# Kernel optimization log

Hardware: AMD Instinct MI355X
Metric: run time of the kernel (lower is better)

## Reference

```python
import jax, jax.numpy as jnp
import numpy as np

B, N, D = 4, 4096, 256


def setup_inputs() -> dict:
    key = jax.random.key(0)
    k1, k2 = jax.random.split(key)
    val = jax.random.normal(k1, (B, N, D), dtype=jnp.float32)
    state = jax.random.normal(k2, (B, N), dtype=jnp.float32)
    return {"val": val, "state": state}


def reference(val, state):
    # pairwise_fn: scaled dot-product -> scores [B, N, N]
    scale = val.shape[-1] ** -0.5
    scores = jnp.einsum("bid,bjd->bij", val, val) * scale
    # edge_compress_fn = softsign (non-softmax compression)
    edges = scores / (1.0 + jnp.abs(scores))
    # state_weight_edges=False, val/state projections are Identity
    delta_state = jnp.einsum("bij,bj->bi", edges, state)   # [B, N]
    delta_val = jnp.einsum("bij,bjd->bid", edges, val)      # [B, N, D]
    return (delta_state, delta_val)
```

## Files before the change

kernel.cpp:

```cpp
#include <hip/hip_runtime.h>


#define B_  4
#define N_  4096
#define D_  256

typedef __attribute__((ext_vector_type(8))) short short8;
typedef __attribute__((ext_vector_type(4))) float floatx4;

__device__ __forceinline__ unsigned short f2bf(float f) {
    unsigned int u = __float_as_uint(f);
    u += 0x7fff + ((u >> 16) & 1);
    return (unsigned short)(u >> 16);
}

__device__ __forceinline__ void gl_lds16(const void* g, void* l) {
    __builtin_amdgcn_global_load_lds(
        (const __attribute__((address_space(1))) unsigned int*)g,
        (__attribute__((address_space(3))) unsigned int*)l, 16, 0, 0);
}
__device__ __forceinline__ void gl_lds4(const void* g, void* l) {
    __builtin_amdgcn_global_load_lds(
        (const __attribute__((address_space(1))) unsigned int*)g,
        (__attribute__((address_space(3))) unsigned int*)l, 4, 0, 0);
}

__global__ __launch_bounds__(256)
void prepass_kernel(const float* __restrict__ val,
                    unsigned short* __restrict__ Vb,
                    unsigned short* __restrict__ VF) {
    __shared__ unsigned short tile[64][68];
    const int t   = threadIdx.x;
    const int blk = blockIdx.x;
    const int b   = blk >> 8;
    const int it  = (blk >> 2) & 63;
    const int dt  = blk & 3;
    const int i0  = it * 64, d0 = dt * 64;
    const float*    vb  = val + (size_t)b * N_ * D_;
    unsigned short* Vbb = Vb  + (size_t)b * N_ * D_;
    unsigned short* VFb = VF  + (size_t)b * N_ * D_;

    #pragma unroll
    for (int q = 0; q < 4; ++q) {
        int idx = t + 256 * q;
        int row = idx >> 4;
        int c4  = idx & 15;
        float4 v = *(const float4*)(vb + (size_t)(i0 + row) * D_ + d0 + c4 * 4);
        ushort4 h;
        h.x = f2bf(v.x); h.y = f2bf(v.y); h.z = f2bf(v.z); h.w = f2bf(v.w);
        *(ushort4*)(Vbb + (size_t)(i0 + row) * D_ + d0 + c4 * 4) = h;
        *(ushort4*)&tile[row][c4 * 4] = h;
    }
    __syncthreads();
    #pragma unroll
    for (int q = 0; q < 4; ++q) {
        int dr = (t >> 4) + q * 16;
        int i4 = t & 15;
        ushort4 h;
        h.x = tile[i4 * 4 + 0][dr];
        h.y = tile[i4 * 4 + 1][dr];
        h.z = tile[i4 * 4 + 2][dr];
        h.w = tile[i4 * 4 + 3][dr];
        const int jb = (i0 >> 5) + (i4 >> 3);
        const int e  = (i4 & 7) * 4;
        *(ushort4*)(VFb + ((size_t)jb * 256 + d0 + dr) * 32 + e) = h;
    }
}

__global__ __launch_bounds__(256, 2)
void prop_main(const float* __restrict__ state,
               const unsigned short* __restrict__ Vb,
               const unsigned short* __restrict__ VF,
               float* __restrict__ dvp,
               float* __restrict__ dsp_o)
{
    __shared__ __attribute__((aligned(16))) unsigned char smem[74752];

    const int t    = threadIdx.x;
    const int w    = t >> 6;
    const int lane = t & 63;
    const int quad = lane >> 4;
    const int l16  = lane & 15;

    const int x   = blockIdx.x;
    const int it  = x >> 3;
    const int b   = (x >> 1) & 3;
    const int jh  = x & 1;
    const int it0 = it * 64;
    const int jbase = jh * 2048;
    const int niter = 32;

    unsigned short* EshL = (unsigned short*)(smem + 65536);
    float*          dsred = (float*)(smem + 74240);

    const unsigned short* Vbb = Vb + (size_t)b * N_ * D_;
    const unsigned short* VFb = VF + (size_t)b * N_ * D_;
    const float*          stb = state + (size_t)b * N_;

    const int hi  = lane >> 5;
    const int p32 = lane & 31;

    int vgoff[8];
    #pragma unroll
    for (int n = 0; n < 8; ++n) {
        int r  = 2 * (w * 8 + n) + hi;
        int gr = p32 ^ (r & 7);
        vgoff[n] = r * 256 + gr * 8;
    }

    const int r0 = (w >> 1) * 32;
    const int c0 = (w & 1) * 32;
    const int pA = l16 & 7;
    const int cB = (w & 1) * 4 + (l16 >> 3);
    const int l7 = l16 & 7;

    const unsigned short* vf_lane = VFb + (size_t)jh * (64 * 8192)
                                  + w * 2048 + l16 * 32 + quad * 8;

    short8 A0[8], A1[8];
    {
        const unsigned short* ar0 = Vbb + (size_t)(it0 + r0 + l16) * 256 + quad * 8;
        const unsigned short* ar1 = ar0 + 16 * 256;
        #pragma unroll
        for (int ks = 0; ks < 8; ++ks) {
            A0[ks] = *(const short8*)(ar0 + ks * 32);
            A1[ks] = *(const short8*)(ar1 + ks * 32);
        }
    }

    #pragma unroll
    for (int n = 0; n < 8; ++n)
        gl_lds16(Vbb + (size_t)jbase * 256 + vgoff[n],
                 smem + (w * 8 + n) * 1024);
    if (w == 0) gl_lds4(stb + jbase + lane, smem + 73728);

    floatx4 dv[4][4];
    #pragma unroll
    for (int a = 0; a < 4; ++a)
        #pragma unroll
        for (int c = 0; c < 4; ++c)
            dv[a][c] = (floatx4){0.f, 0.f, 0.f, 0.f};
    float dsp[8];
    #pragma unroll
    for (int k = 0; k < 8; ++k) dsp[k] = 0.f;

    for (int k = 0; k < niter; ++k) {
        const int buf = k & 1;
        unsigned short* vjL = (unsigned short*)(smem + buf * 32768);
        const float*    stj = (const float*)(smem + 73728 + buf * 256);

        __syncthreads();

        short8 bfr[2][4];
        {
            const unsigned short* vfk = vf_lane + (size_t)k * 16384;
            #pragma unroll
            for (int ks = 0; ks < 2; ++ks)
                #pragma unroll
                for (int c2 = 0; c2 < 4; ++c2)
                    bfr[ks][c2] = *(const short8*)(vfk + ks * 8192 + c2 * 512);
        }

        if (k + 1 < niter) {
            const size_t j0n = jbase + (size_t)(k + 1) * 64;
            #pragma unroll
            for (int n = 0; n < 8; ++n)
                gl_lds16(Vbb + j0n * 256 + vgoff[n],
                         smem + (buf ^ 1) * 32768 + (w * 8 + n) * 1024);
            if (w == 0) gl_lds4(stb + j0n + lane, smem + 73728 + (buf ^ 1) * 256);
        }

        floatx4 sa[2][2];
        #pragma unroll
        for (int a = 0; a < 2; ++a)
            #pragma unroll
            for (int c = 0; c < 2; ++c)
                sa[a][c] = (floatx4){0.f, 0.f, 0.f, 0.f};

        #pragma unroll
        for (int ks = 0; ks < 8; ++ks) {
            const int p = ((ks * 4 + quad) ^ pA) * 8;
            short8 b0 = *(const short8*)&vjL[(c0 + l16) * 256 + p];
            short8 b1 = *(const short8*)&vjL[(c0 + 16 + l16) * 256 + p];
            sa[0][0] = __builtin_amdgcn_mfma_f32_16x16x32_bf16(A0[ks], b0, sa[0][0], 0, 0, 0);
            sa[0][1] = __builtin_amdgcn_mfma_f32_16x16x32_bf16(A0[ks], b1, sa[0][1], 0, 0, 0);
            sa[1][0] = __builtin_amdgcn_mfma_f32_16x16x32_bf16(A1[ks], b0, sa[1][0], 0, 0, 0);
            sa[1][1] = __builtin_amdgcn_mfma_f32_16x16x32_bf16(A1[ks], b1, sa[1][1], 0, 0, 0);
        }

        float stc0 = stj[c0 + l16];
        float stc1 = stj[c0 + 16 + l16];
        #pragma unroll
        for (int a = 0; a < 2; ++a) {
            #pragma unroll
            for (int r = 0; r < 4; ++r) {
                const int il  = r0 + a * 16 + quad * 4 + r;
                const int ilb = (quad * 4 + r) & 7;
                float s0 = sa[a][0][r];
                float s1 = sa[a][1][r];
                float e0 = s0 * __builtin_amdgcn_rcpf(16.0f + fabsf(s0));
                float e1 = s1 * __builtin_amdgcn_rcpf(16.0f + fabsf(s1));
                dsp[a * 4 + r] += e0 * stc0 + e1 * stc1;
                EshL[il * 64 + ((cB ^ ilb) << 3) + l7]       = f2bf(e0);
                EshL[il * 64 + (((cB + 2) ^ ilb) << 3) + l7] = f2bf(e1);
            }
        }
        __syncthreads();

        #pragma unroll
        for (int ks = 0; ks < 2; ++ks) {
            short8 af[4];
            #pragma unroll
            for (int a2 = 0; a2 < 4; ++a2)
                af[a2] = *(const short8*)&EshL[(a2 * 16 + l16) * 64
                                               + (((ks * 4 + quad) ^ l7) << 3)];
            #pragma unroll
            for (int a2 = 0; a2 < 4; ++a2)
                #pragma unroll
                for (int c2 = 0; c2 < 4; ++c2)
                    dv[a2][c2] = __builtin_amdgcn_mfma_f32_16x16x32_bf16(af[a2], bfr[ks][c2], dv[a2][c2], 0, 0, 0);
        }
    }

    float* dvo = dvp + (size_t)jh * B_ * N_ * D_ + (size_t)b * N_ * D_
                     + (size_t)it0 * D_;
    #pragma unroll
    for (int a2 = 0; a2 < 4; ++a2)
        #pragma unroll
        for (int c2 = 0; c2 < 4; ++c2)
            #pragma unroll
            for (int r = 0; r < 4; ++r) {
                const int il = a2 * 16 + quad * 4 + r;
                const int d  = w * 64 + c2 * 16 + l16;
                dvo[(size_t)il * D_ + d] = dv[a2][c2][r];
            }

    #pragma unroll
    for (int k = 0; k < 8; ++k) {
        float v = dsp[k];
        v += __shfl_xor(v, 1);
        v += __shfl_xor(v, 2);
        v += __shfl_xor(v, 4);
        v += __shfl_xor(v, 8);
        dsp[k] = v;
    }
    if (l16 == 0) {
        #pragma unroll
        for (int a = 0; a < 2; ++a)
            #pragma unroll
            for (int r = 0; r < 4; ++r) {
                const int row = r0 + a * 16 + quad * 4 + r;
                dsred[(w & 1) * 64 + row] = dsp[a * 4 + r];
            }
    }
    __syncthreads();
    if (t < 64)
        dsp_o[(size_t)jh * B_ * N_ + (size_t)b * N_ + it0 + t]
            = dsred[t] + dsred[64 + t];
}

__global__ __launch_bounds__(256)
void combine_kernel(const float4* __restrict__ dv0, const float4* __restrict__ dv1,
                    const float*  __restrict__ ds0, const float*  __restrict__ ds1,
                    float* __restrict__ out) {
    const int NDV4 = B_ * N_ * D_ / 4;
    const int NDS  = B_ * N_;
    int x = blockIdx.x * 256 + threadIdx.x;
    if (x < NDV4) {
        float4 a = dv0[x], c = dv1[x];
        float4 r;
        r.x = a.x + c.x; r.y = a.y + c.y; r.z = a.z + c.z; r.w = a.w + c.w;
        ((float4*)(out + NDS))[x] = r;
    } else {
        int y = (x - NDV4) * 4;
        if (y < NDS) {
            float4 a = *(const float4*)(ds0 + y);
            float4 c = *(const float4*)(ds1 + y);
            float4 r;
            r.x = a.x + c.x; r.y = a.y + c.y; r.z = a.z + c.z; r.w = a.w + c.w;
            *(float4*)(out + y) = r;
        }
    }
}

__global__ __launch_bounds__(256, 1)
void prop_kernel_fb(const float* __restrict__ val,
                    const float* __restrict__ state,
                    float* __restrict__ out) {
    __shared__ __attribute__((aligned(16))) unsigned short vi[64][264];
    __shared__ __attribute__((aligned(16))) unsigned short vj[64][264];
    __shared__ __attribute__((aligned(16))) unsigned short vjt[2048][8];
    __shared__ __attribute__((aligned(16))) unsigned short Esh[64][72];
    __shared__ float stj[64];
    __shared__ float dsred[2][64];

    const int t    = threadIdx.x;
    const int w    = t >> 6;
    const int lane = t & 63;
    const int quad = lane >> 4;
    const int l16  = lane & 15;
    const int b   = blockIdx.x >> 6;
    const int it0 = (blockIdx.x & 63) << 6;
    const float* valb = val   + (size_t)b * N_ * D_;
    const float* stb  = state + (size_t)b * N_;

    #pragma unroll
    for (int n = 0; n < 16; ++n) {
        int idx = t + 256 * n;
        int row = idx >> 6;
        int c4  = idx & 63;
        float4 v = *(const float4*)(valb + (size_t)(it0 + row) * D_ + c4 * 4);
        ushort4 h;
        h.x = f2bf(v.x); h.y = f2bf(v.y); h.z = f2bf(v.z); h.w = f2bf(v.w);
        *(ushort4*)&vi[row][c4 * 4] = h;
    }

    const int r0 = (w >> 1) * 32;
    const int c0 = (w & 1) * 32;
    floatx4 dv[4][4];
    #pragma unroll
    for (int a = 0; a < 4; ++a)
        #pragma unroll
        for (int c = 0; c < 4; ++c)
            dv[a][c] = (floatx4){0.f, 0.f, 0.f, 0.f};
    float dsp[8];
    #pragma unroll
    for (int k = 0; k < 8; ++k) dsp[k] = 0.f;

    for (int jt = 0; jt < 64; ++jt) {
        const int j0 = jt * 64;
        #pragma unroll
        for (int n = 0; n < 16; ++n) {
            int idx = t + 256 * n;
            int row = idx >> 6;
            int c4  = idx & 63;
            float4 v = *(const float4*)(valb + (size_t)(j0 + row) * D_ + c4 * 4);
            ushort4 h;
            h.x = f2bf(v.x); h.y = f2bf(v.y); h.z = f2bf(v.z); h.w = f2bf(v.w);
            *(ushort4*)&vj[row][c4 * 4] = h;
        }
        if (t < 64) stj[t] = stb[j0 + t];
        __syncthreads();

        #pragma unroll
        for (int n = 0; n < 8; ++n) {
            const int d  = t;
            const int jb = n;
            short8 pk;
            #pragma unroll
            for (int jj = 0; jj < 8; ++jj) pk[jj] = (short)vj[jb * 8 + jj][d];
            *(short8*)&vjt[d * 8 + (jb ^ (d & 7))][0] = pk;
        }

        floatx4 sa[2][2];
        #pragma unroll
        for (int a = 0; a < 2; ++a)
            #pragma unroll
            for (int c = 0; c < 2; ++c)
                sa[a][c] = (floatx4){0.f, 0.f, 0.f, 0.f};
        #pragma unroll
        for (int ks = 0; ks < 8; ++ks) {
            const int d0 = ks * 32 + quad * 8;
            short8 a0 = *(const short8*)&vi[r0 + l16][d0];
            short8 a1 = *(const short8*)&vi[r0 + 16 + l16][d0];
            short8 b0 = *(const short8*)&vj[c0 + l16][d0];
            short8 b1 = *(const short8*)&vj[c0 + 16 + l16][d0];
            sa[0][0] = __builtin_amdgcn_mfma_f32_16x16x32_bf16(a0, b0, sa[0][0], 0, 0, 0);
            sa[0][1] = __builtin_amdgcn_mfma_f32_16x16x32_bf16(a0, b1, sa[0][1], 0, 0, 0);
            sa[1][0] = __builtin_amdgcn_mfma_f32_16x16x32_bf16(a1, b0, sa[1][0], 0, 0, 0);
            sa[1][1] = __builtin_amdgcn_mfma_f32_16x16x32_bf16(a1, b1, sa[1][1], 0, 0, 0);
        }

        float stc0 = stj[c0 + l16];
        float stc1 = stj[c0 + 16 + l16];
        #pragma unroll
        for (int a = 0; a < 2; ++a) {
            #pragma unroll
            for (int r = 0; r < 4; ++r) {
                const int il = r0 + a * 16 + quad * 4 + r;
                float s0 = sa[a][0][r] * 0.0625f;
                float s1 = sa[a][1][r] * 0.0625f;
                float e0 = s0 / (1.0f + fabsf(s0));
                float e1 = s1 / (1.0f + fabsf(s1));
                dsp[a * 4 + r] += e0 * stc0 + e1 * stc1;
                Esh[il][c0 + l16]      = f2bf(e0);
                Esh[il][c0 + 16 + l16] = f2bf(e1);
            }
        }
        __syncthreads();

        #pragma unroll
        for (int ks = 0; ks < 2; ++ks) {
            short8 af[4], bfr[4];
            #pragma unroll
            for (int a2 = 0; a2 < 4; ++a2)
                af[a2] = *(const short8*)&Esh[a2 * 16 + l16][ks * 32 + quad * 8];
            #pragma unroll
            for (int c2 = 0; c2 < 4; ++c2) {
                const int d  = w * 64 + c2 * 16 + l16;
                const int jb = ks * 4 + quad;
                bfr[c2] = *(const short8*)&vjt[d * 8 + (jb ^ (d & 7))][0];
            }
            #pragma unroll
            for (int a2 = 0; a2 < 4; ++a2)
                #pragma unroll
                for (int c2 = 0; c2 < 4; ++c2)
                    dv[a2][c2] = __builtin_amdgcn_mfma_f32_16x16x32_bf16(af[a2], bfr[c2], dv[a2][c2], 0, 0, 0);
        }
    }

    float* dvo = out + (size_t)B_ * N_ + (size_t)b * N_ * D_;
    #pragma unroll
    for (int a2 = 0; a2 < 4; ++a2)
        #pragma unroll
        for (int c2 = 0; c2 < 4; ++c2)
            #pragma unroll
            for (int r = 0; r < 4; ++r) {
                const int i = it0 + a2 * 16 + quad * 4 + r;
                const int d = w * 64 + c2 * 16 + l16;
                dvo[(size_t)i * D_ + d] = dv[a2][c2][r];
            }

    #pragma unroll
    for (int k = 0; k < 8; ++k) {
        float v = dsp[k];
        v += __shfl_xor(v, 1);
        v += __shfl_xor(v, 2);
        v += __shfl_xor(v, 4);
        v += __shfl_xor(v, 8);
        dsp[k] = v;
    }
    if (l16 == 0) {
        #pragma unroll
        for (int a = 0; a < 2; ++a)
            #pragma unroll
            for (int r = 0; r < 4; ++r) {
                const int row = (w >> 1) * 32 + a * 16 + quad * 4 + r;
                dsred[w & 1][row] = dsp[a * 4 + r];
            }
    }
    __syncthreads();
    if (t < 64) out[(size_t)b * N_ + it0 + t] = dsred[0][t] + dsred[1][t];
}

extern "C" void kernel_launch(void* const* d_in, const int* in_sizes, int n_in,
                              void* d_out, int out_size, void* d_ws, size_t ws_size,
                              hipStream_t stream) {
    const float* val   = (const float*)d_in[0];
    const float* state = (const float*)d_in[1];
    float* out = (float*)d_out;

    const size_t nE         = (size_t)B_ * N_ * D_;
    const size_t need_base  = 2 * nE * sizeof(unsigned short);
    const size_t need_split = need_base + 2 * nE * sizeof(float)
                            + 2 * (size_t)B_ * N_ * sizeof(float);

    if (ws_size >= need_split) {
        unsigned short* Vb = (unsigned short*)d_ws;
        unsigned short* VF = Vb + nE;
        float* dvp = (float*)(VF + nE);
        float* dsp = dvp + 2 * nE;
        prepass_kernel<<<dim3(1024), dim3(256), 0, stream>>>(val, Vb, VF);
        prop_main<<<dim3(512), dim3(256), 0, stream>>>(state, Vb, VF, dvp, dsp);
        const int NDV4 = B_ * N_ * D_ / 4;
        const int NDS4 = B_ * N_ / 4;
        combine_kernel<<<dim3((NDV4 + NDS4) / 256), dim3(256), 0, stream>>>(
            (const float4*)dvp, (const float4*)(dvp + nE),
            dsp, dsp + (size_t)B_ * N_, out);
    } else {
        prop_kernel_fb<<<dim3(256), dim3(256), 0, stream>>>(val, state, out);
    }
}
```

Before: 155.1 us.

## Split j-range into four parts with bf16 partials and single-buffered LDS

The j dimension is split into four quarters instead of two, doubling the grid to 1024 blocks. LDS is cut to a single V buffer plus the edge tile so that four blocks can fit per CU. The V tile prefetch now runs after the edge-write barrier instead of double buffering, and state values are read straight from global memory. Partial dv/ds results are stored as bf16 to halve partial-sum traffic, and the combine kernel sums four bf16 partials. The trade-off is less load/compute overlap within a block and extra rounding error from the bf16 partials.

```diff
diff --git a/kernel.cpp b/kernel.cpp
--- a/kernel.cpp
+++ b/kernel.cpp
@@ -6,6 +6,7 @@
 #define D_  256
 
 typedef __attribute__((ext_vector_type(8))) short short8;
+typedef __attribute__((ext_vector_type(8))) unsigned short ushort8v;
 typedef __attribute__((ext_vector_type(4))) float floatx4;
 
 __device__ __forceinline__ unsigned short f2bf(float f) {
@@ -13,16 +14,14 @@
     u += 0x7fff + ((u >> 16) & 1);
     return (unsigned short)(u >> 16);
 }
+__device__ __forceinline__ float bf2f(unsigned short h) {
+    return __uint_as_float((unsigned int)h << 16);
+}
 
 __device__ __forceinline__ void gl_lds16(const void* g, void* l) {
     __builtin_amdgcn_global_load_lds(
         (const __attribute__((address_space(1))) unsigned int*)g,
         (__attribute__((address_space(3))) unsigned int*)l, 16, 0, 0);
-}
-__device__ __forceinline__ void gl_lds4(const void* g, void* l) {
-    __builtin_amdgcn_global_load_lds(
-        (const __attribute__((address_space(1))) unsigned int*)g,
-        (__attribute__((address_space(3))) unsigned int*)l, 4, 0, 0);
 }
 
 __global__ __launch_bounds__(256)
@@ -67,31 +66,32 @@
     }
 }
 
-__global__ __launch_bounds__(256, 2)
+__global__ __launch_bounds__(256, 4)
 void prop_main(const float* __restrict__ state,
                const unsigned short* __restrict__ Vb,
                const unsigned short* __restrict__ VF,
-               float* __restrict__ dvp,
-               float* __restrict__ dsp_o)
+               unsigned short* __restrict__ dvp,
+               unsigned short* __restrict__ dsp_o)
 {
-    __shared__ __attribute__((aligned(16))) unsigned char smem[74752];
+    __shared__ __attribute__((aligned(16))) unsigned char smem[40960];
 
     const int t    = threadIdx.x;
     const int w    = t >> 6;
     const int lane = t & 63;
     const int quad = lane >> 4;
     const int l16  = lane & 15;
+    const int l7   = lane & 7;
 
     const int x   = blockIdx.x;
-    const int it  = x >> 3;
     const int b   = (x >> 1) & 3;
-    const int jh  = x & 1;
+    const int jq  = (x & 1) * 2 + ((x >> 3) & 1);
+    const int it  = x >> 4;
     const int it0 = it * 64;
-    const int jbase = jh * 2048;
-    const int niter = 32;
-
-    unsigned short* EshL = (unsigned short*)(smem + 65536);
-    float*          dsred = (float*)(smem + 74240);
+    const int jbase = jq * 1024;
+    const int niter = 16;
+
+    unsigned short* vjL  = (unsigned short*)smem;
+    unsigned short* EshL = (unsigned short*)(smem + 32768);
 
     const unsigned short* Vbb = Vb + (size_t)b * N_ * D_;
     const unsigned short* VFb = VF + (size_t)b * N_ * D_;
@@ -110,12 +110,10 @@
 
     const int r0 = (w >> 1) * 32;
     const int c0 = (w & 1) * 32;
-    const int pA = l16 & 7;
     const int cB = (w & 1) * 4 + (l16 >> 3);
-    const int l7 = l16 & 7;
-
-    const unsigned short* vf_lane = VFb + (size_t)jh * (64 * 8192)
-                                  + w * 2048 + l16 * 32 + quad * 8;
+
+    const unsigned short* vf_lane = VFb + (size_t)jq * 32 * 8192
+                                  + (w * 64 + l16) * 32 + quad * 8;
 
     short8 A0[8], A1[8];
     {
@@ -132,7 +130,6 @@
     for (int n = 0; n < 8; ++n)
         gl_lds16(Vbb + (size_t)jbase * 256 + vgoff[n],
                  smem + (w * 8 + n) * 1024);
-    if (w == 0) gl_lds4(stb + jbase + lane, smem + 73728);
 
     floatx4 dv[4][4];
     #pragma unroll
@@ -145,11 +142,11 @@
     for (int k = 0; k < 8; ++k) dsp[k] = 0.f;
 
     for (int k = 0; k < niter; ++k) {
-        const int buf = k & 1;
-        unsigned short* vjL = (unsigned short*)(smem + buf * 32768);
-        const float*    stj = (const float*)(smem + 73728 + buf * 256);
-
         __syncthreads();
+
+        const int j0 = jbase + k * 64;
+        float stc0 = stb[j0 + c0 + l16];
+        float stc1 = stb[j0 + c0 + 16 + l16];
 
         short8 bfr[2][4];
         {
@@ -161,15 +158,6 @@
                     bfr[ks][c2] = *(const short8*)(vfk + ks * 8192 + c2 * 512);
         }
 
-        if (k + 1 < niter) {
-            const size_t j0n = jbase + (size_t)(k + 1) * 64;
-            #pragma unroll
-            for (int n = 0; n < 8; ++n)
-                gl_lds16(Vbb + j0n * 256 + vgoff[n],
-                         smem + (buf ^ 1) * 32768 + (w * 8 + n) * 1024);
-            if (w == 0) gl_lds4(stb + j0n + lane, smem + 73728 + (buf ^ 1) * 256);
-        }
-
         floatx4 sa[2][2];
         #pragma unroll
         for (int a = 0; a < 2; ++a)
@@ -179,7 +167,7 @@
 
         #pragma unroll
         for (int ks = 0; ks < 8; ++ks) {
-            const int p = ((ks * 4 + quad) ^ pA) * 8;
+            const int p = ((ks * 4 + quad) ^ l7) * 8;
             short8 b0 = *(const short8*)&vjL[(c0 + l16) * 256 + p];
             short8 b1 = *(const short8*)&vjL[(c0 + 16 + l16) * 256 + p];
             sa[0][0] = __builtin_amdgcn_mfma_f32_16x16x32_bf16(A0[ks], b0, sa[0][0], 0, 0, 0);
@@ -188,8 +176,6 @@
             sa[1][1] = __builtin_amdgcn_mfma_f32_16x16x32_bf16(A1[ks], b1, sa[1][1], 0, 0, 0);
         }
 
-        float stc0 = stj[c0 + l16];
-        float stc1 = stj[c0 + 16 + l16];
         #pragma unroll
         for (int a = 0; a < 2; ++a) {
             #pragma unroll
@@ -207,6 +193,14 @@
         }
         __syncthreads();
 
+        if (k + 1 < niter) {
+            const size_t j0n = (size_t)(jbase + (k + 1) * 64);
+            #pragma unroll
+            for (int n = 0; n < 8; ++n)
+                gl_lds16(Vbb + j0n * 256 + vgoff[n],
+                         smem + (w * 8 + n) * 1024);
+        }
+
         #pragma unroll
         for (int ks = 0; ks < 2; ++ks) {
             short8 af[4];
@@ -222,8 +216,8 @@
         }
     }
 
-    float* dvo = dvp + (size_t)jh * B_ * N_ * D_ + (size_t)b * N_ * D_
-                     + (size_t)it0 * D_;
+    unsigned short* dvo = dvp + ((size_t)jq * B_ + b) * N_ * D_
+                        + (size_t)it0 * D_;
     #pragma unroll
     for (int a2 = 0; a2 < 4; ++a2)
         #pragma unroll
@@ -232,9 +226,10 @@
             for (int r = 0; r < 4; ++r) {
                 const int il = a2 * 16 + quad * 4 + r;
                 const int d  = w * 64 + c2 * 16 + l16;
-                dvo[(size_t)il * D_ + d] = dv[a2][c2][r];
-            }
-
+                dvo[(size_t)il * D_ + d] = f2bf(dv[a2][c2][r]);
+            }
+
+    float* dsred = (float*)smem;
     #pragma unroll
     for (int k = 0; k < 8; ++k) {
         float v = dsp[k];
@@ -255,29 +250,44 @@
     }
     __syncthreads();
     if (t < 64)
-        dsp_o[(size_t)jh * B_ * N_ + (size_t)b * N_ + it0 + t]
-            = dsred[t] + dsred[64 + t];
+        dsp_o[(size_t)jq * B_ * N_ + (size_t)b * N_ + it0 + t]
+            = f2bf(dsred[t] + dsred[64 + t]);
 }
 
 __global__ __launch_bounds__(256)
-void combine_kernel(const float4* __restrict__ dv0, const float4* __restrict__ dv1,
-                    const float*  __restrict__ ds0, const float*  __restrict__ ds1,
+void combine_kernel(const unsigned short* __restrict__ dvp,
+                    const unsigned short* __restrict__ dsp,
                     float* __restrict__ out) {
-    const int NDV4 = B_ * N_ * D_ / 4;
-    const int NDS  = B_ * N_;
+    const size_t nE  = (size_t)B_ * N_ * D_;
+    const int  NDV8  = B_ * N_ * D_ / 8;
+    const int  NDS   = B_ * N_;
     int x = blockIdx.x * 256 + threadIdx.x;
-    if (x < NDV4) {
-        float4 a = dv0[x], c = dv1[x];
-        float4 r;
-        r.x = a.x + c.x; r.y = a.y + c.y; r.z = a.z + c.z; r.w = a.w + c.w;
-        ((float4*)(out + NDS))[x] = r;
+    if (x < NDV8) {
+        float acc[8];
+        #pragma unroll
+        for (int i = 0; i < 8; ++i) acc[i] = 0.f;
+        #pragma unroll
+        for (int q = 0; q < 4; ++q) {
+            ushort8v v = *(const ushort8v*)(dvp + q * nE + (size_t)x * 8);
+            #pragma unroll
+            for (int i = 0; i < 8; ++i) acc[i] += bf2f(v[i]);
+        }
+        float4 r0, r1;
+        r0.x = acc[0]; r0.y = acc[1]; r0.z = acc[2]; r0.w = acc[3];
+        r1.x = acc[4]; r1.y = acc[5]; r1.z = acc[6]; r1.w = acc[7];
+        *(float4*)(out + NDS + (size_t)x * 8)     = r0;
+        *(float4*)(out + NDS + (size_t)x * 8 + 4) = r1;
     } else {
-        int y = (x - NDV4) * 4;
+        int y = (x - NDV8) * 4;
         if (y < NDS) {
-            float4 a = *(const float4*)(ds0 + y);
-            float4 c = *(const float4*)(ds1 + y);
-            float4 r;
-            r.x = a.x + c.x; r.y = a.y + c.y; r.z = a.z + c.z; r.w = a.w + c.w;
+            float a0 = 0.f, a1 = 0.f, a2 = 0.f, a3 = 0.f;
+            #pragma unroll
+            for (int q = 0; q < 4; ++q) {
+                ushort4 v = *(const ushort4*)(dsp + q * NDS + y);
+                a0 += bf2f(v.x); a1 += bf2f(v.y);
+                a2 += bf2f(v.z); a3 += bf2f(v.w);
+            }
+            float4 r; r.x = a0; r.y = a1; r.z = a2; r.w = a3;
             *(float4*)(out + y) = r;
         }
     }
@@ -451,22 +461,21 @@
     float* out = (float*)d_out;
 
     const size_t nE         = (size_t)B_ * N_ * D_;
-    const size_t need_base  = 2 * nE * sizeof(unsigned short);
-    const size_t need_split = need_base + 2 * nE * sizeof(float)
-                            + 2 * (size_t)B_ * N_ * sizeof(float);
+    const size_t need_split = 2 * nE * sizeof(unsigned short)
+                            + 4 * nE * sizeof(unsigned short)
+                            + 4 * (size_t)B_ * N_ * sizeof(unsigned short);
 
     if (ws_size >= need_split) {
-        unsigned short* Vb = (unsigned short*)d_ws;
-        unsigned short* VF = Vb + nE;
-        float* dvp = (float*)(VF + nE);
-        float* dsp = dvp + 2 * nE;
+        unsigned short* Vb  = (unsigned short*)d_ws;
+        unsigned short* VF  = Vb + nE;
+        unsigned short* dvp = VF + nE;
+        unsigned short* dsp = dvp + 4 * nE;
         prepass_kernel<<<dim3(1024), dim3(256), 0, stream>>>(val, Vb, VF);
-        prop_main<<<dim3(512), dim3(256), 0, stream>>>(state, Vb, VF, dvp, dsp);
-        const int NDV4 = B_ * N_ * D_ / 4;
+        prop_main<<<dim3(1024), dim3(256), 0, stream>>>(state, Vb, VF, dvp, dsp);
+        const int NDV8 = B_ * N_ * D_ / 8;
         const int NDS4 = B_ * N_ / 4;
-        combine_kernel<<<dim3((NDV4 + NDS4) / 256), dim3(256), 0, stream>>>(
-            (const float4*)dvp, (const float4*)(dvp + nE),
-            dsp, dsp + (size_t)B_ * N_, out);
+        combine_kernel<<<dim3((NDV8 + NDS4 + 255) / 256), dim3(256), 0, stream>>>(
+            dvp, dsp, out);
     } else {
         prop_kernel_fb<<<dim3(256), dim3(256), 0, stream>>>(val, state, out);
     }
```

Result: slower. 393.9 us (+154.0%).
